# Optimization experiments

Hardware: AMD Instinct MI355X
Metric: run time of the kernel (lower is better)

The kernel has to match this reference:

```python
import jax, jax.numpy as jnp
import numpy as np

N, E, G = 40000, 400000, 40
DIN, DH, DOUT = 128, 256, 128
NEG_SLOPE = 0.2  # PyG GATConv default leaky_relu slope


def _gat_layer(h_in, src, dst, W, a_src, a_dst, b, num_nodes):
    # h_in: [N, din]; src/dst: [E'] (self loops included); W: [din, dout]
    h = h_in @ W                                   # [N, dout]
    al_s = h @ a_src                               # [N]
    al_d = h @ a_dst                               # [N]
    e = jax.nn.leaky_relu(al_s[src] + al_d[dst], NEG_SLOPE)  # [E']
    # scatter-softmax over incoming edges of each dst node (stable)
    m = jax.ops.segment_max(e, dst, num_segments=num_nodes)
    ex = jnp.exp(e - m[dst])
    denom = jax.ops.segment_sum(ex, dst, num_segments=num_nodes)
    alpha = ex / denom[dst]                        # [E']
    out = jax.ops.segment_sum(h[src] * alpha[:, None], dst, num_segments=num_nodes)
    return out + b


def setup_inputs() -> dict:
    key = jax.random.key(0)
    ks = jax.random.split(key, 16)
    x = jax.random.normal(ks[0], (N, DIN), dtype=jnp.float32)
    edge_index = jax.random.randint(ks[1], (2, E), 0, N, dtype=jnp.int64)

    def lin(k, din, dout):
        return jax.random.normal(k, (din, dout), dtype=jnp.float32) / np.sqrt(din)

    def vec(k, d):
        return jax.random.normal(k, (d,), dtype=jnp.float32) / np.sqrt(d)

    return dict(
        x=x, edge_index=edge_index, num_graphs=G,
        W1=lin(ks[2], DIN, DH), a_src1=vec(ks[3], DH), a_dst1=vec(ks[4], DH), b1=jnp.zeros((DH,), jnp.float32),
        W2=lin(ks[5], DH, DH), a_src2=vec(ks[6], DH), a_dst2=vec(ks[7], DH), b2=jnp.zeros((DH,), jnp.float32),
        W3=lin(ks[8], DH, DOUT), a_src3=vec(ks[9], DOUT), a_dst3=vec(ks[10], DOUT), b3=jnp.zeros((DOUT,), jnp.float32),
    )


def reference(x, edge_index, num_graphs, W1, a_src1, a_dst1, b1, W2, a_src2, a_dst2, b2, W3, a_src3, a_dst3, b3):
    num_nodes = x.shape[0]
    # PyG GATConv adds self-loops by default
    loop = jnp.arange(num_nodes, dtype=edge_index.dtype)
    src = jnp.concatenate([edge_index[0], loop])
    dst = jnp.concatenate([edge_index[1], loop])

    h = jax.nn.relu(_gat_layer(x, src, dst, W1, a_src1, a_dst1, b1, num_nodes))
    # dropout is identity in eval mode
    h = jax.nn.relu(_gat_layer(h, src, dst, W2, a_src2, a_dst2, b2, num_nodes))
    h = _gat_layer(h, src, dst, W3, a_src3, a_dst3, b3, num_nodes)
    return h.reshape(num_graphs, num_nodes // num_graphs, -1)
```

## Files before the change

### kernel.cpp

```cpp
#include <hip/hip_runtime.h>
#include <hip/hip_bf16.h>
#include <type_traits>

typedef __attribute__((ext_vector_type(8))) short short8;
typedef __attribute__((ext_vector_type(4))) float f32x4;
typedef __attribute__((ext_vector_type(2))) float f32x2;
typedef __attribute__((ext_vector_type(4))) unsigned short u16x4;
typedef __attribute__((ext_vector_type(2))) unsigned short u16x2;

static __device__ __forceinline__ unsigned short f2b(float f) {
    unsigned int v = __float_as_uint(f);
    unsigned int r = (v + 0x7FFFu + ((v >> 16) & 1u)) >> 16;
    return (unsigned short)r;
}
static __device__ __forceinline__ float b2f(unsigned short u) {
    return __uint_as_float(((unsigned int)u) << 16);
}

template<int V> struct FVec;
template<> struct FVec<4> { using T = f32x4; };
template<> struct FVec<2> { using T = f32x2; };
template<int V> struct UVec;
template<> struct UVec<4> { using T = u16x4; };
template<> struct UVec<2> { using T = u16x2; };

__global__ void k_init_cnt(int* cnt, int* cursor, int n) {
    int i = blockIdx.x * 256 + threadIdx.x;
    if (i < n) cnt[i] = 1;
    if (i == 0) *cursor = 0;
}

__global__ void k_hist(const int* __restrict__ dst, int* __restrict__ cnt, int E) {
    int e = blockIdx.x * 256 + threadIdx.x;
    if (e < E) atomicAdd(&cnt[dst[e]], 1);
}

__global__ void k_assign(const int* __restrict__ cnt, int* __restrict__ begptr,
                         int* __restrict__ colidx, int* __restrict__ fill,
                         int* __restrict__ cursor, int n) {
    int i = blockIdx.x * 256 + threadIdx.x;
    int lane = threadIdx.x & 63;
    int c = (i < n) ? cnt[i] : 0;
    int s = c;
#pragma unroll
    for (int off = 1; off < 64; off <<= 1) {
        int v = __shfl_up(s, off);
        if (lane >= off) s += v;
    }
    int wavesum = __shfl(s, 63);
    int base = 0;
    if (lane == 63) base = atomicAdd(cursor, wavesum);
    base = __shfl(base, 63);
    int beg = base + s - c;
    if (i < n) { begptr[i] = beg; colidx[beg] = i; fill[i] = 1; }
}

__global__ void k_scatter(const int* __restrict__ src, const int* __restrict__ dst,
                          const int* __restrict__ begptr, int* __restrict__ fill,
                          int* __restrict__ colidx, int E) {
    int e = blockIdx.x * 256 + threadIdx.x;
    if (e < E) {
        int s = src[e], d = dst[e];
        int pos = atomicAdd(&fill[d], 1);
        colidx[begptr[d] + pos] = s;
    }
}

__global__ void k_transpose(const float* __restrict__ w, unsigned short* __restrict__ wt,
                            int K, int Nc) {
    int i = blockIdx.x * 256 + threadIdx.x;
    if (i < K * Nc) {
        int k = i / Nc, n = i % Nc;
        wt[n * K + k] = f2b(w[i]);
    }
}

template<int NC, typename AT>
__global__ __launch_bounds__(256) void k_gemm(const AT* __restrict__ A,
                                              const unsigned short* __restrict__ Bt,
                                              unsigned short* __restrict__ H,
                                              const float* __restrict__ asrc,
                                              const float* __restrict__ adst,
                                              float* __restrict__ als,
                                              float* __restrict__ ald,
                                              int K) {
    __shared__ unsigned short As[64][40];
    __shared__ unsigned short Bs[NC][40];
    const int tid  = threadIdx.x;
    const int lane = tid & 63;
    const int wv   = tid >> 6;
    const int rowBase = blockIdx.x * 64;
    const int quad = lane >> 4;
    const int l16  = lane & 15;
    constexpr int NT = NC / 16;
    f32x4 acc[NT] = {};

    const int ar = tid >> 2;
    const int ak = (tid & 3) * 8;

    for (int kk = 0; kk < K; kk += 32) {
        if constexpr (std::is_same_v<AT, float>) {
            const float* ap = A + (size_t)(rowBase + ar) * K + kk + ak;
            f32x4 a0 = *(const f32x4*)ap;
            f32x4 a1 = *(const f32x4*)(ap + 4);
            short8 s;
#pragma unroll
            for (int v = 0; v < 4; v++) { s[v] = (short)f2b(a0[v]); s[4 + v] = (short)f2b(a1[v]); }
            *(short8*)&As[ar][ak] = s;
        } else {
            *(short8*)&As[ar][ak] = *(const short8*)(A + (size_t)(rowBase + ar) * K + kk + ak);
        }
#pragma unroll
        for (int c = tid; c < NC * 4; c += 256) {
            int br = c >> 2, bk = (c & 3) * 8;
            *(short8*)&Bs[br][bk] = *(const short8*)(Bt + (size_t)br * K + kk + bk);
        }
        __syncthreads();
        short8 af = *(const short8*)&As[wv * 16 + l16][quad * 8];
#pragma unroll
        for (int nt = 0; nt < NT; nt++) {
            short8 bf = *(const short8*)&Bs[nt * 16 + l16][quad * 8];
            acc[nt] = __builtin_amdgcn_mfma_f32_16x16x32_bf16(af, bf, acc[nt], 0, 0, 0);
        }
        __syncthreads();
    }

    float avs[NT], avd[NT];
#pragma unroll
    for (int nt = 0; nt < NT; nt++) {
        int gcol = nt * 16 + l16;
        avs[nt] = asrc[gcol];
        avd[nt] = adst[gcol];
#pragma unroll
        for (int r = 0; r < 4; r++) {
            int grow = rowBase + wv * 16 + quad * 4 + r;
            H[(size_t)grow * NC + gcol] = f2b(acc[nt][r]);
        }
    }
#pragma unroll
    for (int r = 0; r < 4; r++) {
        float ps = 0.f, pd = 0.f;
#pragma unroll
        for (int nt = 0; nt < NT; nt++) { ps += acc[nt][r] * avs[nt]; pd += acc[nt][r] * avd[nt]; }
#pragma unroll
        for (int off = 8; off; off >>= 1) { ps += __shfl_xor(ps, off); pd += __shfl_xor(pd, off); }
        if (l16 == 0) {
            int grow = rowBase + wv * 16 + quad * 4 + r;
            als[grow] = ps;
            ald[grow] = pd;
        }
    }
}

template<int DOUT, bool RELU, typename OutT>
__global__ __launch_bounds__(256) void k_edge(const unsigned short* __restrict__ h,
                                              const float* __restrict__ als,
                                              const float* __restrict__ ald,
                                              const int* __restrict__ begptr,
                                              const int* __restrict__ cnt,
                                              const int* __restrict__ colidx,
                                              const float* __restrict__ bias,
                                              OutT* __restrict__ out, int N) {
    int node = blockIdx.x * 4 + (threadIdx.x >> 6);
    if (node >= N) return;
    int lane = threadIdx.x & 63;
    int beg = begptr[node];
    int deg = cnt[node];
    float aldi = ald[node];

    float m = -1e30f;
    float e_lane = -1e30f;
    int   s_lane = 0;
    for (int j = lane; j < deg; j += 64) {
        int s = colidx[beg + j];
        float e = als[s] + aldi;
        e = e > 0.f ? e : 0.2f * e;
        if (j < 64) { e_lane = e; s_lane = s; }
        m = fmaxf(m, e);
    }
#pragma unroll
    for (int off = 32; off; off >>= 1) m = fmaxf(m, __shfl_xor(m, off));

    float dsum = (lane < deg) ? __expf(e_lane - m) : 0.f;
    for (int j = lane + 64; j < deg; j += 64) {
        int s = colidx[beg + j];
        float e = als[s] + aldi;
        e = e > 0.f ? e : 0.2f * e;
        dsum += __expf(e - m);
    }
#pragma unroll
    for (int off = 32; off; off >>= 1) dsum += __shfl_xor(dsum, off);
    float inv = 1.0f / dsum;
    float w_lane = (lane < deg) ? __expf(e_lane - m) * inv : 0.f;

    constexpr int V = DOUT / 64;
    using UT = typename UVec<V>::T;
    float acc[V] = {};
    int lim = deg < 64 ? deg : 64;
    const size_t laneOff = (size_t)lane * V;
    for (int j = 0; j < lim; j++) {
        float wj = __shfl(w_lane, j);
        int   sj = __shfl(s_lane, j);
        UT hv = *(const UT*)(h + (size_t)sj * DOUT + laneOff);
#pragma unroll
        for (int v = 0; v < V; v++) acc[v] += wj * b2f(hv[v]);
    }
    for (int j = 64; j < deg; j++) {
        int sj = colidx[beg + j];
        float e = als[sj] + aldi;
        e = e > 0.f ? e : 0.2f * e;
        float wj = __expf(e - m) * inv;
        UT hv = *(const UT*)(h + (size_t)sj * DOUT + laneOff);
#pragma unroll
        for (int v = 0; v < V; v++) acc[v] += wj * b2f(hv[v]);
    }

    typename FVec<V>::T bv = *(const typename FVec<V>::T*)(bias + laneOff);
    if constexpr (std::is_same_v<OutT, float>) {
        typename FVec<V>::T ov;
#pragma unroll
        for (int v = 0; v < V; v++) {
            float val = acc[v] + bv[v];
            if (RELU) val = fmaxf(val, 0.f);
            ov[v] = val;
        }
        *(typename FVec<V>::T*)(out + (size_t)node * DOUT + laneOff) = ov;
    } else {
        UT ov;
#pragma unroll
        for (int v = 0; v < V; v++) {
            float val = acc[v] + bv[v];
            if (RELU) val = fmaxf(val, 0.f);
            ov[v] = f2b(val);
        }
        *(UT*)(out + (size_t)node * DOUT + laneOff) = ov;
    }
}

extern "C" void kernel_launch(void* const* d_in, const int* in_sizes, int n_in,
                              void* d_out, int out_size, void* d_ws, size_t ws_size,
                              hipStream_t stream) {
    const int DIN = 128, DH = 256, DOUT = 128;
    const int N = in_sizes[0] / DIN;
    const int E = in_sizes[1] / 2;

    const float* x   = (const float*)d_in[0];
    const int*   ei  = (const int*)d_in[1];
    const float* W1  = (const float*)d_in[3];
    const float* as1 = (const float*)d_in[4];
    const float* ad1 = (const float*)d_in[5];
    const float* b1  = (const float*)d_in[6];
    const float* W2  = (const float*)d_in[7];
    const float* as2 = (const float*)d_in[8];
    const float* ad2 = (const float*)d_in[9];
    const float* b2  = (const float*)d_in[10];
    const float* W3  = (const float*)d_in[11];
    const float* as3 = (const float*)d_in[12];
    const float* ad3 = (const float*)d_in[13];
    const float* b3  = (const float*)d_in[14];
    float* outp = (float*)d_out;

    char* ws = (char*)d_ws;
    size_t off = 0;
    auto carve = [&](size_t bytes) { char* p = ws + off; off = (off + bytes + 255) & ~(size_t)255; return p; };
    unsigned short* hbuf = (unsigned short*)carve((size_t)N * DH * 2);
    unsigned short* gbuf = (unsigned short*)carve((size_t)N * DH * 2);
    float* als  = (float*)carve((size_t)N * 4);
    float* ald  = (float*)carve((size_t)N * 4);
    unsigned short* wt = (unsigned short*)carve((size_t)DH * DH * 2);
    int* cnt    = (int*)carve((size_t)N * 4);
    int* begptr = (int*)carve((size_t)N * 4);
    int* fill   = (int*)carve((size_t)N * 4);
    int* cursor = (int*)carve(256);
    int* colidx = (int*)carve((size_t)(E + N) * 4);
    (void)ws_size; (void)n_in; (void)out_size;

    const int* e_src = ei;
    const int* e_dst = ei + E;

    k_init_cnt<<<(N + 255) / 256, 256, 0, stream>>>(cnt, cursor, N);
    k_hist<<<(E + 255) / 256, 256, 0, stream>>>(e_dst, cnt, E);
    k_assign<<<(N + 255) / 256, 256, 0, stream>>>(cnt, begptr, colidx, fill, cursor, N);
    k_scatter<<<(E + 255) / 256, 256, 0, stream>>>(e_src, e_dst, begptr, fill, colidx, E);

    const int nblk4 = (N + 3) / 4;
    const int mblk  = N / 64;

    k_transpose<<<(DIN * DH + 255) / 256, 256, 0, stream>>>(W1, wt, DIN, DH);
    k_gemm<256, float><<<mblk, 256, 0, stream>>>(x, wt, hbuf, as1, ad1, als, ald, DIN);
    k_edge<256, true, unsigned short><<<nblk4, 256, 0, stream>>>(hbuf, als, ald, begptr, cnt, colidx, b1, gbuf, N);

    k_transpose<<<(DH * DH + 255) / 256, 256, 0, stream>>>(W2, wt, DH, DH);
    k_gemm<256, unsigned short><<<mblk, 256, 0, stream>>>(gbuf, wt, hbuf, as2, ad2, als, ald, DH);
    k_edge<256, true, unsigned short><<<nblk4, 256, 0, stream>>>(hbuf, als, ald, begptr, cnt, colidx, b2, gbuf, N);

    k_transpose<<<(DH * DOUT + 255) / 256, 256, 0, stream>>>(W3, wt, DH, DOUT);
    k_gemm<128, unsigned short><<<mblk, 256, 0, stream>>>(gbuf, wt, hbuf, as3, ad3, als, ald, DH);
    k_edge<128, false, float><<<nblk4, 256, 0, stream>>>(hbuf, als, ald, begptr, cnt, colidx, b3, outp, N);
}
```

Baseline: 332.0 us.

## Split aggregation wave into four quarter-groups processing edges in parallel

The edge-aggregation loop now splits each 64-lane wave into four 16-lane groups. Each group handles a different neighbor edge at a time and loads 16-byte bf16 vectors covering a wider slice of the feature row. Partial sums are then combined with cross-lane xor shuffles, and only the first quarter writes the output. This aims to raise memory-level parallelism and use wider loads for low-degree nodes, at the cost of more registers per lane and a reduction step. Edges beyond 64 are handled serially by quarter 0 alone.

```diff
diff --git a/kernel.cpp b/kernel.cpp
--- a/kernel.cpp
+++ b/kernel.cpp
@@ -5,8 +5,7 @@
 typedef __attribute__((ext_vector_type(8))) short short8;
 typedef __attribute__((ext_vector_type(4))) float f32x4;
 typedef __attribute__((ext_vector_type(2))) float f32x2;
-typedef __attribute__((ext_vector_type(4))) unsigned short u16x4;
-typedef __attribute__((ext_vector_type(2))) unsigned short u16x2;
+typedef __attribute__((ext_vector_type(8))) unsigned short u16x8;
 
 static __device__ __forceinline__ unsigned short f2b(float f) {
     unsigned int v = __float_as_uint(f);
@@ -16,13 +15,6 @@
 static __device__ __forceinline__ float b2f(unsigned short u) {
     return __uint_as_float(((unsigned int)u) << 16);
 }
-
-template<int V> struct FVec;
-template<> struct FVec<4> { using T = f32x4; };
-template<> struct FVec<2> { using T = f32x2; };
-template<int V> struct UVec;
-template<> struct UVec<4> { using T = u16x4; };
-template<> struct UVec<2> { using T = u16x2; };
 
 __global__ void k_init_cnt(int* cnt, int* cursor, int n) {
     int i = blockIdx.x * 256 + threadIdx.x;
@@ -193,47 +185,76 @@
     float inv = 1.0f / dsum;
     float w_lane = (lane < deg) ? __expf(e_lane - m) * inv : 0.f;
 
-    constexpr int V = DOUT / 64;
-    using UT = typename UVec<V>::T;
-    float acc[V] = {};
+    constexpr int QV  = DOUT / 16;
+    constexpr int NC8 = QV / 8;
+    const int l16g    = lane & 15;
+    const int quarter = lane >> 4;
+    const size_t dimOff = (size_t)l16g * QV;
+    float acc[QV] = {};
     int lim = deg < 64 ? deg : 64;
-    const size_t laneOff = (size_t)lane * V;
-    for (int j = 0; j < lim; j++) {
-        float wj = __shfl(w_lane, j);
-        int   sj = __shfl(s_lane, j);
-        UT hv = *(const UT*)(h + (size_t)sj * DOUT + laneOff);
-#pragma unroll
-        for (int v = 0; v < V; v++) acc[v] += wj * b2f(hv[v]);
+    for (int t = 0; 4 * t < lim; t++) {
+        int idx = 4 * t + quarter;
+        float wj = __shfl(w_lane, idx);
+        int   sj = __shfl(s_lane, idx);
+        const unsigned short* hp = h + (size_t)sj * DOUT + dimOff;
+        u16x8 c[NC8];
+#pragma unroll
+        for (int u = 0; u < NC8; u++) c[u] = *(const u16x8*)(hp + 8 * u);
+#pragma unroll
+        for (int u = 0; u < NC8; u++)
+#pragma unroll
+            for (int v = 0; v < 8; v++) acc[8 * u + v] += wj * b2f(c[u][v]);
     }
     for (int j = 64; j < deg; j++) {
         int sj = colidx[beg + j];
         float e = als[sj] + aldi;
         e = e > 0.f ? e : 0.2f * e;
         float wj = __expf(e - m) * inv;
-        UT hv = *(const UT*)(h + (size_t)sj * DOUT + laneOff);
-#pragma unroll
-        for (int v = 0; v < V; v++) acc[v] += wj * b2f(hv[v]);
-    }
-
-    typename FVec<V>::T bv = *(const typename FVec<V>::T*)(bias + laneOff);
-    if constexpr (std::is_same_v<OutT, float>) {
-        typename FVec<V>::T ov;
-#pragma unroll
-        for (int v = 0; v < V; v++) {
-            float val = acc[v] + bv[v];
-            if (RELU) val = fmaxf(val, 0.f);
-            ov[v] = val;
-        }
-        *(typename FVec<V>::T*)(out + (size_t)node * DOUT + laneOff) = ov;
-    } else {
-        UT ov;
-#pragma unroll
-        for (int v = 0; v < V; v++) {
-            float val = acc[v] + bv[v];
-            if (RELU) val = fmaxf(val, 0.f);
-            ov[v] = f2b(val);
-        }
-        *(UT*)(out + (size_t)node * DOUT + laneOff) = ov;
+        if (quarter == 0) {
+            const unsigned short* hp = h + (size_t)sj * DOUT + dimOff;
+#pragma unroll
+            for (int u = 0; u < NC8; u++) {
+                u16x8 c = *(const u16x8*)(hp + 8 * u);
+#pragma unroll
+                for (int v = 0; v < 8; v++) acc[8 * u + v] += wj * b2f(c[v]);
+            }
+        }
+    }
+#pragma unroll
+    for (int v = 0; v < QV; v++) {
+        acc[v] += __shfl_xor(acc[v], 16);
+        acc[v] += __shfl_xor(acc[v], 32);
+    }
+
+    if (quarter == 0) {
+        if constexpr (std::is_same_v<OutT, float>) {
+            float* op = out + (size_t)node * DOUT + dimOff;
+#pragma unroll
+            for (int u = 0; u < QV / 4; u++) {
+                f32x4 bv = *(const f32x4*)(bias + dimOff + 4 * u);
+                f32x4 ov;
+#pragma unroll
+                for (int v = 0; v < 4; v++) {
+                    float val = acc[4 * u + v] + bv[v];
+                    if (RELU) val = fmaxf(val, 0.f);
+                    ov[v] = val;
+                }
+                *(f32x4*)(op + 4 * u) = ov;
+            }
+        } else {
+            unsigned short* op = out + (size_t)node * DOUT + dimOff;
+#pragma unroll
+            for (int u = 0; u < NC8; u++) {
+                u16x8 ov;
+#pragma unroll
+                for (int v = 0; v < 8; v++) {
+                    float val = acc[8 * u + v] + bias[dimOff + 8 * u + v];
+                    if (RELU) val = fmaxf(val, 0.f);
+                    ov[v] = f2b(val);
+                }
+                *(u16x8*)(op + 8 * u) = ov;
+            }
+        }
     }
 }
 
```

After: 302.5 us. 1.1x faster.
